# Kernel optimization log

Measured on AMD Instinct MI355X. Metric: run time of the kernel, lower is better.

Reference implementation:

```python
import jax, jax.numpy as jnp
import numpy as np

# TT-linear: in_features=1024 -> out_features=4096
IN_DIMS = (8, 8, 4, 4)      # m1..m4, prod = 1024
OUT_DIMS = (8, 8, 8, 8)     # n1..n4, prod = 4096
RANKS = (1, 16, 16, 16, 1)  # r0..r4
IN_FEATURES = 1024
OUT_FEATURES = 4096
BATCH, SEQ = 4, 1024


def _init_core(key, shape):
    # uniform(-1,1)/sqrt(fan_in-ish), matching the original's uniform-style init scale
    fan = shape[0] * shape[1]
    return (2.0 * jax.random.uniform(key, shape, dtype=jnp.float32) - 1.0) / np.sqrt(fan).astype(np.float32)


def setup_inputs() -> dict:
    key = jax.random.key(0)
    ks = jax.random.split(key, 6)
    x = jax.random.normal(ks[0], (BATCH, SEQ, IN_FEATURES), dtype=jnp.float32)
    core0 = _init_core(ks[1], (1, 8, 8, 16))    # [r0, m1, n1, r1]
    core1 = _init_core(ks[2], (16, 8, 8, 16))   # [r1, m2, n2, r2]
    core2 = _init_core(ks[3], (16, 4, 8, 16))   # [r2, m3, n3, r3]
    core3 = _init_core(ks[4], (16, 4, 8, 1))    # [r3, m4, n4, r4]
    bias = (2.0 * jax.random.uniform(ks[5], (OUT_FEATURES,), dtype=jnp.float32) - 1.0) / np.sqrt(OUT_FEATURES).astype(np.float32)
    return {"x": x, "core0": core0, "core1": core1, "core2": core2, "core3": core3, "bias": bias}


def reference(x, core0, core1, core2, core3, bias):
    lead = x.shape[:-1]
    # split the feature axis into TT input factors: [T, m1, m2, m3, m4]
    t = x.reshape((-1,) + IN_DIMS)
    c0 = core0[0]        # [m1, n1, r1]   (boundary rank r0 = 1 squeezed)
    c3 = core3[..., 0]   # [r3, m4, n4]   (boundary rank r4 = 1 squeezed)
    # sequential TT core chain: absorb one m_k, emit one n_k per step
    t = jnp.einsum('tijkl,ixp->tjklxp', t, c0)      # [T, m2,m3,m4, n1, r1]
    t = jnp.einsum('tjklxp,pjyq->tklxyq', t, core1)  # [T, m3,m4, n1,n2, r2]
    t = jnp.einsum('tklxyq,qkzr->tlxyzr', t, core2)  # [T, m4, n1,n2,n3, r3]
    t = jnp.einsum('tlxyzr,rlw->txyzw', t, c3)       # [T, n1,n2,n3,n4]
    y = t.reshape(lead + (OUT_FEATURES,)) + bias
    return y
```

## Files before the change

### kernel.cpp

```cpp
#include <hip/hip_runtime.h>
#include <hip/hip_bf16.h>
#include <cstdint>


typedef __bf16 bf16x8 __attribute__((ext_vector_type(8)));
typedef float f32x4 __attribute__((ext_vector_type(4)));

__device__ __forceinline__ void g2lds16(const void* g, void* l) {
    __builtin_amdgcn_global_load_lds(
        (const __attribute__((address_space(1))) void*)g,
        (__attribute__((address_space(3))) void*)l,
        16, 0, 0);
}

__global__ __launch_bounds__(256) void prep(
    const float* __restrict__ x, __bf16* __restrict__ xb,
    const float* __restrict__ c0, const float* __restrict__ c1,
    const float* __restrict__ c2, const float* __restrict__ c3,
    __bf16* __restrict__ wt) {
    const int b = blockIdx.x;
    const int t = threadIdx.x;
    if (b < 2048) {
        const int i = (b * 256 + t) * 8;
        float4 a0 = *(const float4*)(x + i);
        float4 a1 = *(const float4*)(x + i + 4);
        bf16x8 o;
        o[0] = (__bf16)a0.x; o[1] = (__bf16)a0.y; o[2] = (__bf16)a0.z; o[3] = (__bf16)a0.w;
        o[4] = (__bf16)a1.x; o[5] = (__bf16)a1.y; o[6] = (__bf16)a1.z; o[7] = (__bf16)a1.w;
        *(bf16x8*)(xb + i) = o;
        return;
    }
    __shared__ float t12[4][16];
    __shared__ float t123[4][512];
    __shared__ float c3s[512];
    #pragma unroll
    for (int i = t; i < 512; i += 256) c3s[i] = c3[i];
    const int s = t >> 6;
    const int lane = t & 63;
    const int g = (b - 2048) * 4 + s;
    const int m1 = g >> 9, n1 = (g >> 6) & 7, m2 = (g >> 3) & 7, n2 = g & 7;
    __syncthreads();
    if (lane < 16) {
        const int r2 = lane;
        float sum = 0.f;
        #pragma unroll
        for (int r1 = 0; r1 < 16; ++r1)
            sum += c0[(m1 * 8 + n1) * 16 + r1] * c1[((r1 * 8 + m2) * 8 + n2) * 16 + r2];
        t12[s][r2] = sum;
    }
    __syncthreads();
    #pragma unroll
    for (int idx = lane; idx < 512; idx += 64) {
        const int m3 = idx >> 7, n3 = (idx >> 4) & 7, r3 = idx & 15;
        float sum = 0.f;
        #pragma unroll
        for (int r2 = 0; r2 < 16; ++r2)
            sum += t12[s][r2] * c2[((r2 * 4 + m3) * 8 + n3) * 16 + r3];
        t123[s][(m3 * 8 + n3) * 16 + r3] = sum;
    }
    __syncthreads();
    const int n3 = lane >> 3, n4 = lane & 7;
    const int n = ((n1 * 8 + n2) * 8 + n3) * 8 + n4;
    const int kbase = (m1 * 8 + m2) * 16;
    float v[16];
    #pragma unroll
    for (int e = 0; e < 16; ++e) v[e] = 0.f;
    #pragma unroll
    for (int m3 = 0; m3 < 4; ++m3) {
        #pragma unroll
        for (int r3 = 0; r3 < 16; ++r3) {
            const float tv = t123[s][(m3 * 8 + n3) * 16 + r3];
            #pragma unroll
            for (int m4 = 0; m4 < 4; ++m4)
                v[m3 * 4 + m4] += tv * c3s[(r3 * 4 + m4) * 8 + n4];
        }
    }
    bf16x8 lo, hi;
    #pragma unroll
    for (int e = 0; e < 8; ++e) { lo[e] = (__bf16)v[e]; hi[e] = (__bf16)v[8 + e]; }
    *(bf16x8*)(wt + (size_t)n * 1024 + kbase)     = lo;
    *(bf16x8*)(wt + (size_t)n * 1024 + kbase + 8) = hi;
}


#define SCHED_FENCE() __builtin_amdgcn_sched_barrier(0)
#define BARRIER() do { SCHED_FENCE(); __builtin_amdgcn_s_barrier(); SCHED_FENCE(); } while (0)
#define VMCNT(n)  do { SCHED_FENCE(); asm volatile("s_waitcnt vmcnt(" #n ")"); SCHED_FENCE(); } while (0)

__global__ __launch_bounds__(512, 2) void tt_gemm(
    const __bf16* __restrict__ A, const __bf16* __restrict__ B,
    const float* __restrict__ bias, float* __restrict__ C) {
    constexpr int K = 1024, N = 4096;
    constexpr int NT = K / 32;
    __shared__ __bf16 sA[4][256 * 32];
    __shared__ __bf16 sB[4][256 * 32];
    const int t = threadIdx.x;
    const int lane = t & 63;
    const int wave = t >> 6;
    const int wm = (wave >> 2) * 128;
    const int wn = (wave & 3) * 64;
    const int l15 = lane & 15, lh = lane >> 4;
    const int coff = (lh ^ ((l15 >> 1) & 3)) * 16;

    const int xcd = blockIdx.x & 7;
    const int lid = blockIdx.x >> 3;
    const int bm = ((xcd >> 2) * 8 + (lid & 7)) * 256;
    const int bn = ((xcd & 3) * 4 + (lid >> 3)) * 256;

    const int c0i = t, c1i = t + 512;
    const int r0 = c0i >> 2, r1 = c1i >> 2;
    const int lc0 = (c0i & 3) ^ ((r0 >> 1) & 3);
    const int lc1 = (c1i & 3) ^ ((r1 >> 1) & 3);
    const __bf16* a0p = A + (size_t)(bm + r0) * K + lc0 * 8;
    const __bf16* a1p = A + (size_t)(bm + r1) * K + lc1 * 8;
    const __bf16* b0p = B + (size_t)(bn + r0) * K + lc0 * 8;
    const __bf16* b1p = B + (size_t)(bn + r1) * K + lc1 * 8;

#define STAGE_A(kt) do { \
    g2lds16(a0p + (kt) * 32, (char*)sA[(kt) & 3] + c0i * 16); \
    g2lds16(a1p + (kt) * 32, (char*)sA[(kt) & 3] + c1i * 16); } while (0)
#define STAGE_B(kt) do { \
    g2lds16(b0p + (kt) * 32, (char*)sB[(kt) & 3] + c0i * 16); \
    g2lds16(b1p + (kt) * 32, (char*)sB[(kt) & 3] + c1i * 16); } while (0)

    f32x4 acc[8][4] = {};

    STAGE_A(0); STAGE_B(0);
    STAGE_A(1); STAGE_B(1);
    STAGE_A(2); STAGE_B(2);
    VMCNT(8);
    BARRIER();

    #pragma unroll 1
    for (int kt = 0; kt < NT - 3; ++kt) {
        const char* la = (const char*)sA[kt & 3];
        const char* lb = (const char*)sB[kt & 3];
        bf16x8 af[4], bfr[4];
        #pragma unroll
        for (int mi = 0; mi < 4; ++mi)
            af[mi] = *(const bf16x8*)(la + (wm + mi * 16 + l15) * 64 + coff);
        #pragma unroll
        for (int ni = 0; ni < 4; ++ni)
            bfr[ni] = *(const bf16x8*)(lb + (wn + ni * 16 + l15) * 64 + coff);
        STAGE_A(kt + 3);
        BARRIER();
        __builtin_amdgcn_s_setprio(1);
        #pragma unroll
        for (int mi = 0; mi < 4; ++mi)
            #pragma unroll
            for (int ni = 0; ni < 4; ++ni)
                acc[mi][ni] = __builtin_amdgcn_mfma_f32_16x16x32_bf16(
                    af[mi], bfr[ni], acc[mi][ni], 0, 0, 0);
        __builtin_amdgcn_s_setprio(0);
        BARRIER();
        #pragma unroll
        for (int mi = 0; mi < 4; ++mi)
            af[mi] = *(const bf16x8*)(la + (wm + 64 + mi * 16 + l15) * 64 + coff);
        STAGE_B(kt + 3);
        VMCNT(8);
        BARRIER();
        __builtin_amdgcn_s_setprio(1);
        #pragma unroll
        for (int mi = 0; mi < 4; ++mi)
            #pragma unroll
            for (int ni = 0; ni < 4; ++ni)
                acc[4 + mi][ni] = __builtin_amdgcn_mfma_f32_16x16x32_bf16(
                    af[mi], bfr[ni], acc[4 + mi][ni], 0, 0, 0);
        __builtin_amdgcn_s_setprio(0);
        BARRIER();
    }

    VMCNT(0);
    BARRIER();
    #pragma unroll
    for (int kt = NT - 3; kt < NT; ++kt) {
        const char* la = (const char*)sA[kt & 3];
        const char* lb = (const char*)sB[kt & 3];
        bf16x8 af[4], bfr[4];
        #pragma unroll
        for (int ni = 0; ni < 4; ++ni)
            bfr[ni] = *(const bf16x8*)(lb + (wn + ni * 16 + l15) * 64 + coff);
        #pragma unroll
        for (int mi = 0; mi < 4; ++mi)
            af[mi] = *(const bf16x8*)(la + (wm + mi * 16 + l15) * 64 + coff);
        #pragma unroll
        for (int mi = 0; mi < 4; ++mi)
            #pragma unroll
            for (int ni = 0; ni < 4; ++ni)
                acc[mi][ni] = __builtin_amdgcn_mfma_f32_16x16x32_bf16(
                    af[mi], bfr[ni], acc[mi][ni], 0, 0, 0);
        #pragma unroll
        for (int mi = 0; mi < 4; ++mi)
            af[mi] = *(const bf16x8*)(la + (wm + 64 + mi * 16 + l15) * 64 + coff);
        #pragma unroll
        for (int mi = 0; mi < 4; ++mi)
            #pragma unroll
            for (int ni = 0; ni < 4; ++ni)
                acc[4 + mi][ni] = __builtin_amdgcn_mfma_f32_16x16x32_bf16(
                    af[mi], bfr[ni], acc[4 + mi][ni], 0, 0, 0);
    }

    #pragma unroll
    for (int ni = 0; ni < 4; ++ni) {
        const int col = bn + wn + ni * 16 + l15;
        const float bv = bias[col];
        #pragma unroll
        for (int mi = 0; mi < 8; ++mi) {
            const int row0 = bm + wm + mi * 16 + lh * 4;
            const f32x4 v = acc[mi][ni];
            #pragma unroll
            for (int r = 0; r < 4; ++r)
                C[(size_t)(row0 + r) * N + col] = v[r] + bv;
        }
    }
#undef STAGE_A
#undef STAGE_B
}

extern "C" void kernel_launch(void* const* d_in, const int* in_sizes, int n_in,
                              void* d_out, int out_size, void* d_ws, size_t ws_size,
                              hipStream_t stream) {
    const float* x    = (const float*)d_in[0];
    const float* c0   = (const float*)d_in[1];
    const float* c1   = (const float*)d_in[2];
    const float* c2   = (const float*)d_in[3];
    const float* c3   = (const float*)d_in[4];
    const float* bias = (const float*)d_in[5];
    float* out = (float*)d_out;

    __bf16* xb = (__bf16*)d_ws;
    __bf16* wt = xb + (size_t)4096 * 1024;

    prep<<<3072, 256, 0, stream>>>(x, xb, c0, c1, c2, c3, wt);
    tt_gemm<<<256, 512, 0, stream>>>(xb, wt, bias, out);
}
```

Baseline: 148.8 us.

## Collapse GEMM main loop to one barrier per K-tile with merged staging

Replaces the split two-phase main loop, which used four barriers per K-tile and interleaved A/B staging with half-tile MFMA groups, with one phase per tile. Each phase issues both A and B prefetches for tile kt+3, loads all eight A fragments and four B fragments, runs 32 MFMAs, then does a single vmcnt wait and barrier. The tail is peeled with explicit vmcnt(4), vmcnt(0) waits. The epilogue is reordered so stores iterate row-major with bias hoisted. The aim is less barrier overhead; the cost is higher register pressure from eight live A fragments, and having only one barrier per tile means the 4-buffer ring must still keep tile kt+3 from overwriting a buffer other waves are still reading.

```diff
diff --git a/kernel.cpp b/kernel.cpp
--- a/kernel.cpp
+++ b/kernel.cpp
@@ -84,8 +84,6 @@
 
 
 #define SCHED_FENCE() __builtin_amdgcn_sched_barrier(0)
-#define BARRIER() do { SCHED_FENCE(); __builtin_amdgcn_s_barrier(); SCHED_FENCE(); } while (0)
-#define VMCNT(n)  do { SCHED_FENCE(); asm volatile("s_waitcnt vmcnt(" #n ")"); SCHED_FENCE(); } while (0)
 
 __global__ __launch_bounds__(512, 2) void tt_gemm(
     const __bf16* __restrict__ A, const __bf16* __restrict__ B,
@@ -123,98 +121,76 @@
     g2lds16(b0p + (kt) * 32, (char*)sB[(kt) & 3] + c0i * 16); \
     g2lds16(b1p + (kt) * 32, (char*)sB[(kt) & 3] + c1i * 16); } while (0)
 
+#define TILE_COMPUTE(kt) do {                                                  \
+    const char* la = (const char*)sA[(kt) & 3];                                \
+    const char* lb = (const char*)sB[(kt) & 3];                                \
+    bf16x8 af[8], bfr[4];                                                      \
+    _Pragma("unroll")                                                          \
+    for (int mi = 0; mi < 8; ++mi)                                             \
+        af[mi] = *(const bf16x8*)(la + (wm + mi * 16 + l15) * 64 + coff);      \
+    _Pragma("unroll")                                                          \
+    for (int ni = 0; ni < 4; ++ni)                                             \
+        bfr[ni] = *(const bf16x8*)(lb + (wn + ni * 16 + l15) * 64 + coff);     \
+    __builtin_amdgcn_s_setprio(1);                                             \
+    _Pragma("unroll")                                                          \
+    for (int mi = 0; mi < 8; ++mi)                                             \
+        _Pragma("unroll")                                                      \
+        for (int ni = 0; ni < 4; ++ni)                                         \
+            acc[mi][ni] = __builtin_amdgcn_mfma_f32_16x16x32_bf16(             \
+                af[mi], bfr[ni], acc[mi][ni], 0, 0, 0);                        \
+    __builtin_amdgcn_s_setprio(0);                                             \
+} while (0)
+
     f32x4 acc[8][4] = {};
 
     STAGE_A(0); STAGE_B(0);
     STAGE_A(1); STAGE_B(1);
     STAGE_A(2); STAGE_B(2);
-    VMCNT(8);
-    BARRIER();
+    SCHED_FENCE();
+    asm volatile("s_waitcnt vmcnt(8)");
+    SCHED_FENCE();
+    __builtin_amdgcn_s_barrier();
+    SCHED_FENCE();
 
     #pragma unroll 1
     for (int kt = 0; kt < NT - 3; ++kt) {
-        const char* la = (const char*)sA[kt & 3];
-        const char* lb = (const char*)sB[kt & 3];
-        bf16x8 af[4], bfr[4];
-        #pragma unroll
-        for (int mi = 0; mi < 4; ++mi)
-            af[mi] = *(const bf16x8*)(la + (wm + mi * 16 + l15) * 64 + coff);
-        #pragma unroll
-        for (int ni = 0; ni < 4; ++ni)
-            bfr[ni] = *(const bf16x8*)(lb + (wn + ni * 16 + l15) * 64 + coff);
-        STAGE_A(kt + 3);
-        BARRIER();
-        __builtin_amdgcn_s_setprio(1);
-        #pragma unroll
-        for (int mi = 0; mi < 4; ++mi)
+        STAGE_A(kt + 3); STAGE_B(kt + 3);
+        TILE_COMPUTE(kt);
+        SCHED_FENCE();
+        asm volatile("s_waitcnt vmcnt(8)");
+        __builtin_amdgcn_s_barrier();
+        SCHED_FENCE();
+    }
+
+    TILE_COMPUTE(NT - 3);
+    SCHED_FENCE();
+    asm volatile("s_waitcnt vmcnt(4)");
+    __builtin_amdgcn_s_barrier();
+    SCHED_FENCE();
+    TILE_COMPUTE(NT - 2);
+    SCHED_FENCE();
+    asm volatile("s_waitcnt vmcnt(0)");
+    __builtin_amdgcn_s_barrier();
+    SCHED_FENCE();
+    TILE_COMPUTE(NT - 1);
+
+    float bv[4];
+    #pragma unroll
+    for (int ni = 0; ni < 4; ++ni) bv[ni] = bias[bn + wn + ni * 16 + l15];
+    #pragma unroll
+    for (int mi = 0; mi < 8; ++mi) {
+        #pragma unroll
+        for (int r = 0; r < 4; ++r) {
+            const int row = bm + wm + mi * 16 + lh * 4 + r;
+            float* crow = C + (size_t)row * N + bn + wn + l15;
             #pragma unroll
             for (int ni = 0; ni < 4; ++ni)
-                acc[mi][ni] = __builtin_amdgcn_mfma_f32_16x16x32_bf16(
-                    af[mi], bfr[ni], acc[mi][ni], 0, 0, 0);
-        __builtin_amdgcn_s_setprio(0);
-        BARRIER();
-        #pragma unroll
-        for (int mi = 0; mi < 4; ++mi)
-            af[mi] = *(const bf16x8*)(la + (wm + 64 + mi * 16 + l15) * 64 + coff);
-        STAGE_B(kt + 3);
-        VMCNT(8);
-        BARRIER();
-        __builtin_amdgcn_s_setprio(1);
-        #pragma unroll
-        for (int mi = 0; mi < 4; ++mi)
-            #pragma unroll
-            for (int ni = 0; ni < 4; ++ni)
-                acc[4 + mi][ni] = __builtin_amdgcn_mfma_f32_16x16x32_bf16(
-                    af[mi], bfr[ni], acc[4 + mi][ni], 0, 0, 0);
-        __builtin_amdgcn_s_setprio(0);
-        BARRIER();
-    }
-
-    VMCNT(0);
-    BARRIER();
-    #pragma unroll
-    for (int kt = NT - 3; kt < NT; ++kt) {
-        const char* la = (const char*)sA[kt & 3];
-        const char* lb = (const char*)sB[kt & 3];
-        bf16x8 af[4], bfr[4];
-        #pragma unroll
-        for (int ni = 0; ni < 4; ++ni)
-            bfr[ni] = *(const bf16x8*)(lb + (wn + ni * 16 + l15) * 64 + coff);
-        #pragma unroll
-        for (int mi = 0; mi < 4; ++mi)
-            af[mi] = *(const bf16x8*)(la + (wm + mi * 16 + l15) * 64 + coff);
-        #pragma unroll
-        for (int mi = 0; mi < 4; ++mi)
-            #pragma unroll
-            for (int ni = 0; ni < 4; ++ni)
-                acc[mi][ni] = __builtin_amdgcn_mfma_f32_16x16x32_bf16(
-                    af[mi], bfr[ni], acc[mi][ni], 0, 0, 0);
-        #pragma unroll
-        for (int mi = 0; mi < 4; ++mi)
-            af[mi] = *(const bf16x8*)(la + (wm + 64 + mi * 16 + l15) * 64 + coff);
-        #pragma unroll
-        for (int mi = 0; mi < 4; ++mi)
-            #pragma unroll
-            for (int ni = 0; ni < 4; ++ni)
-                acc[4 + mi][ni] = __builtin_amdgcn_mfma_f32_16x16x32_bf16(
-                    af[mi], bfr[ni], acc[4 + mi][ni], 0, 0, 0);
-    }
-
-    #pragma unroll
-    for (int ni = 0; ni < 4; ++ni) {
-        const int col = bn + wn + ni * 16 + l15;
-        const float bv = bias[col];
-        #pragma unroll
-        for (int mi = 0; mi < 8; ++mi) {
-            const int row0 = bm + wm + mi * 16 + lh * 4;
-            const f32x4 v = acc[mi][ni];
-            #pragma unroll
-            for (int r = 0; r < 4; ++r)
-                C[(size_t)(row0 + r) * N + col] = v[r] + bv;
+                crow[ni * 16] = acc[mi][ni][r] + bv[ni];
         }
     }
 #undef STAGE_A
 #undef STAGE_B
+#undef TILE_COMPUTE
 }
 
 extern "C" void kernel_launch(void* const* d_in, const int* in_sizes, int n_in,
```

New measurement: 144.0 us. 1.03x faster.
